# Performance work log

Hardware: AMD Instinct MI355X
Metric: run time of the kernel (lower is better)

The kernel has to match this reference:

```python
import jax, jax.numpy as jnp
import numpy as np

RADIUS = 0.2
NSAMPLE = 32
USE_XYZ = True


def setup_inputs() -> dict:
    key = jax.random.key(0)
    k1, k2, k3 = jax.random.split(key, 3)
    B, N, S, C = 8, 16384, 1024, 64
    xyz = jax.random.uniform(k1, (B, N, 3), dtype=jnp.float32)
    new_xyz = jax.random.uniform(k2, (B, S, 3), dtype=jnp.float32)
    features = jax.random.normal(k3, (B, C, N), dtype=jnp.float32)
    return {"xyz": xyz, "new_xyz": new_xyz, "features": features}


def _ball_query(xyz, new_xyz, radius, nsample):
    """For each query point, the first `nsample` point indices within `radius`,
    padded with the first valid index (0 if none) — matches the CUDA kernel."""
    B, N, _ = xyz.shape
    # squared distances [B, S, N]
    d2 = jnp.sum((new_xyz[:, :, None, :] - xyz[:, None, :, :]) ** 2, axis=-1)
    within = d2 < (radius * radius)
    # encode: valid points keep their index, invalid get sentinel N; sorting
    # then yields the first-in-order valid indices, as the CUDA kernel does.
    keys = jnp.where(within, jnp.arange(N, dtype=jnp.int32)[None, None, :], N)
    idx = jnp.sort(keys, axis=-1)[:, :, :nsample]          # [B, S, K]
    first = idx[:, :, 0:1]
    first = jnp.where(first < N, first, 0)                 # no neighbor -> 0
    idx = jnp.where(idx < N, idx, first)
    return idx.astype(jnp.int32)


def reference(xyz, new_xyz, features):
    idx = _ball_query(xyz, new_xyz, RADIUS, NSAMPLE)       # [B, S, K] int32
    # group xyz: gather [B, S, K, 3] then center on new_xyz
    grouped_xyz = jnp.take_along_axis(xyz[:, None, :, :], idx[:, :, :, None], axis=2)
    grouped_xyz = grouped_xyz - new_xyz[:, :, None, :]
    grouped_xyz = jnp.transpose(grouped_xyz, (0, 3, 1, 2))  # [B, 3, S, K]
    # group features: [B, C, 1, N] gathered with [B, 1, S, K] -> [B, C, S, K]
    grouped_feats = jnp.take_along_axis(features[:, :, :, None].transpose(0, 1, 3, 2),
                                        idx[:, None, :, :], axis=3)
    if USE_XYZ:
        return jnp.concatenate([grouped_xyz, grouped_feats], axis=1)  # [B, 3+C, S, K]
    return grouped_feats
```

## Files before the change

kernel.cpp:

```cpp
#include <hip/hip_runtime.h>


#define BB 8
#define NN 16384
#define SS 1024
#define CC 64
#define NSAMP 32
#define OUTCH (3 + CC)

#define R2 0.04f

__global__ __launch_bounds__(256) void query_kernel(
    const float* __restrict__ xyz,
    const float* __restrict__ new_xyz,
    int* __restrict__ idxq,
    float* __restrict__ out)
{
    __shared__ int sidx[4][NSAMP];

    const int t    = threadIdx.x;
    const int wave = t >> 6;
    const int lane = t & 63;
    const int q    = blockIdx.x * 4 + wave;
    const int b    = q >> 10;
    const int s    = q & (SS - 1);

    const float* xb = xyz + (size_t)b * NN * 3;
    const float qx = new_xyz[((size_t)b * SS + s) * 3 + 0];
    const float qy = new_xyz[((size_t)b * SS + s) * 3 + 1];
    const float qz = new_xyz[((size_t)b * SS + s) * 3 + 2];
    const unsigned long long below = (1ull << lane) - 1ull;

    int count = 0;
    for (int base = 0; base < NN; base += 512) {
        float d2[8];
        #pragma unroll
        for (int j = 0; j < 8; ++j) {
            const int i = base + j * 64 + lane;
            const float dx = qx - xb[i * 3 + 0];
            const float dy = qy - xb[i * 3 + 1];
            const float dz = qz - xb[i * 3 + 2];
            d2[j] = __fadd_rn(__fadd_rn(__fmul_rn(dx, dx),
                                        __fmul_rn(dy, dy)),
                              __fmul_rn(dz, dz));
        }
        #pragma unroll
        for (int j = 0; j < 8; ++j) {
            const bool within = d2[j] < R2;
            const unsigned long long m = __ballot(within);
            if (within) {
                const int pos = count + __popcll(m & below);
                if (pos < NSAMP) sidx[wave][pos] = base + j * 64 + lane;
            }
            count += __popcll(m);
        }
        if (count >= NSAMP) break;
    }
    __syncthreads();
    const int cnt = count < NSAMP ? count : NSAMP;
    const int first = (cnt > 0) ? sidx[wave][0] : 0;
    if (lane < NSAMP && lane >= cnt) sidx[wave][lane] = first;
    __syncthreads();

    if (lane < NSAMP) {
        const int k = lane;
        const int idx = sidx[wave][k];
        idxq[(size_t)q * NSAMP + k] = idx;
        const float gx = xb[idx * 3 + 0] - qx;
        const float gy = xb[idx * 3 + 1] - qy;
        const float gz = xb[idx * 3 + 2] - qz;
        const size_t o = (((size_t)b * OUTCH + 0) * SS + s) * NSAMP + k;
        out[o + 0 * (size_t)SS * NSAMP] = gx;
        out[o + 1 * (size_t)SS * NSAMP] = gy;
        out[o + 2 * (size_t)SS * NSAMP] = gz;
    }
}

__global__ __launch_bounds__(512) void gather_kernel(
    const float* __restrict__ feats,
    const int*   __restrict__ idxq,
    float* __restrict__ out)
{
    __shared__ float row[NN];

    const int c = blockIdx.x;
    const int b = blockIdx.y;
    const int t = threadIdx.x;

    const float* fr = feats + ((size_t)b * CC + c) * NN;
    #pragma unroll
    for (int i = 0; i < 8; ++i) {
        const int o = (i * 512 + t) * 4;
        *(float4*)(row + o) = *(const float4*)(fr + o);
    }
    __syncthreads();

    const int k4 = (t & 7) * 4;
    const int s0 = t >> 3;
    const int*  ib = idxq + (size_t)b * SS * NSAMP;
    float* ob = out + (((size_t)b * OUTCH + 3 + c) * SS) * NSAMP;
    #pragma unroll
    for (int it = 0; it < 16; ++it) {
        const int s = it * 64 + s0;
        const int4 id = *(const int4*)(ib + (size_t)s * NSAMP + k4);
        float4 v;
        v.x = row[id.x];
        v.y = row[id.y];
        v.z = row[id.z];
        v.w = row[id.w];
        *(float4*)(ob + (size_t)s * NSAMP + k4) = v;
    }
}

__global__ __launch_bounds__(64) void qg_fused(
    const float* __restrict__ xyz, const float* __restrict__ new_xyz,
    const float* __restrict__ feats, float* __restrict__ out)
{
    const int bs   = blockIdx.x;
    const int b    = bs >> 10;
    const int s    = bs & (SS - 1);
    const int lane = threadIdx.x;

    const float* xb = xyz + (size_t)b * NN * 3;
    const float qx = new_xyz[((size_t)b * SS + s) * 3 + 0];
    const float qy = new_xyz[((size_t)b * SS + s) * 3 + 1];
    const float qz = new_xyz[((size_t)b * SS + s) * 3 + 2];

    __shared__ int sidx[NSAMP];
    int count = 0;
    for (int base = 0; base < NN; base += 64) {
        const int i = base + lane;
        const float dx = qx - xb[i * 3 + 0];
        const float dy = qy - xb[i * 3 + 1];
        const float dz = qz - xb[i * 3 + 2];
        const float d2 = __fadd_rn(__fadd_rn(__fmul_rn(dx, dx),
                                             __fmul_rn(dy, dy)),
                                   __fmul_rn(dz, dz));
        const bool within = d2 < R2;
        const unsigned long long m = __ballot(within);
        if (within) {
            const int pos = count + __popcll(m & ((1ull << lane) - 1ull));
            if (pos < NSAMP) sidx[pos] = i;
        }
        count += __popcll(m);
        if (count >= NSAMP) break;
    }
    __syncthreads();
    const int cnt = count < NSAMP ? count : NSAMP;
    const int first = (cnt > 0) ? sidx[0] : 0;
    if (lane < NSAMP && lane >= cnt) sidx[lane] = first;
    __syncthreads();

    const int k    = lane & 31;
    const int half = lane >> 5;
    const int idx  = sidx[k];
    const size_t obase = (((size_t)b * OUTCH + 0) * SS + s) * NSAMP + k;
    if (half == 0) {
        out[obase + 0 * (size_t)SS * NSAMP] = xb[idx * 3 + 0] - qx;
        out[obase + 1 * (size_t)SS * NSAMP] = xb[idx * 3 + 1] - qy;
        out[obase + 2 * (size_t)SS * NSAMP] = xb[idx * 3 + 2] - qz;
    }
    const float* fb = feats + (size_t)b * CC * NN;
    const size_t fo = (((size_t)b * OUTCH + 3) * SS + s) * NSAMP + k;
    for (int cch = half; cch < CC; cch += 2) {
        out[fo + (size_t)cch * SS * NSAMP] = fb[(size_t)cch * NN + idx];
    }
}

extern "C" void kernel_launch(void* const* d_in, const int* in_sizes, int n_in,
                              void* d_out, int out_size, void* d_ws, size_t ws_size,
                              hipStream_t stream) {
    const float* xyz     = (const float*)d_in[0];
    const float* new_xyz = (const float*)d_in[1];
    const float* feats   = (const float*)d_in[2];
    float* out           = (float*)d_out;

    const size_t idx_bytes = (size_t)BB * SS * NSAMP * sizeof(int);

    if (ws_size >= idx_bytes) {
        int* idxq = (int*)d_ws;
        query_kernel<<<2048, 256, 0, stream>>>(xyz, new_xyz, idxq, out);
        gather_kernel<<<dim3(CC, BB), 512, 0, stream>>>(feats, idxq, out);
    } else {
        qg_fused<<<BB * SS, 64, 0, stream>>>(xyz, new_xyz, feats, out);
    }
}
```

Measured before the change: 115.4 us.

## Fuse ball query and feature gather into one kernel with per-batch atomic barrier

Merges the query and gather kernels into a single launch of 512 blocks. Each block first computes 16 ball queries for its batch while its feature row loads into registers, then signals a per-batch atomic counter and spin-waits until all 64 blocks of that batch finish before gathering. If the wait times out, the block recomputes all queries itself as a fallback. This drops one kernel launch and overlaps the feature loads with the query work. It relies on all blocks of a batch being co-resident, adds a memset and spin-wait cost, and swaps the popcount prefix for mbcnt.

```diff
diff --git a/kernel.cpp b/kernel.cpp
--- a/kernel.cpp
+++ b/kernel.cpp
@@ -7,30 +7,19 @@
 #define CC 64
 #define NSAMP 32
 #define OUTCH (3 + CC)
+#define GPB 64
+#define QPG 16
 
 #define R2 0.04f
 
-__global__ __launch_bounds__(256) void query_kernel(
-    const float* __restrict__ xyz,
-    const float* __restrict__ new_xyz,
+__device__ __forceinline__ void ball_query_one(
+    const float* __restrict__ xb,
+    const float qx, const float qy, const float qz,
+    const int b, const int s, const int lane,
+    int* __restrict__ swave,
     int* __restrict__ idxq,
     float* __restrict__ out)
 {
-    __shared__ int sidx[4][NSAMP];
-
-    const int t    = threadIdx.x;
-    const int wave = t >> 6;
-    const int lane = t & 63;
-    const int q    = blockIdx.x * 4 + wave;
-    const int b    = q >> 10;
-    const int s    = q & (SS - 1);
-
-    const float* xb = xyz + (size_t)b * NN * 3;
-    const float qx = new_xyz[((size_t)b * SS + s) * 3 + 0];
-    const float qy = new_xyz[((size_t)b * SS + s) * 3 + 1];
-    const float qz = new_xyz[((size_t)b * SS + s) * 3 + 2];
-    const unsigned long long below = (1ull << lane) - 1ull;
-
     int count = 0;
     for (int base = 0; base < NN; base += 512) {
         float d2[8];
@@ -49,23 +38,26 @@
             const bool within = d2[j] < R2;
             const unsigned long long m = __ballot(within);
             if (within) {
-                const int pos = count + __popcll(m & below);
-                if (pos < NSAMP) sidx[wave][pos] = base + j * 64 + lane;
+                const int pre = (int)__builtin_amdgcn_mbcnt_hi(
+                    (unsigned)(m >> 32),
+                    __builtin_amdgcn_mbcnt_lo((unsigned)m, 0u));
+                const int pos = count + pre;
+                if (pos < NSAMP) swave[pos] = base + j * 64 + lane;
             }
             count += __popcll(m);
         }
         if (count >= NSAMP) break;
     }
-    __syncthreads();
+    asm volatile("s_waitcnt lgkmcnt(0)" ::: "memory");
     const int cnt = count < NSAMP ? count : NSAMP;
-    const int first = (cnt > 0) ? sidx[wave][0] : 0;
-    if (lane < NSAMP && lane >= cnt) sidx[wave][lane] = first;
-    __syncthreads();
+    const int first = (cnt > 0) ? swave[0] : 0;
+    if (lane < NSAMP && lane >= cnt) swave[lane] = first;
+    asm volatile("s_waitcnt lgkmcnt(0)" ::: "memory");
 
     if (lane < NSAMP) {
         const int k = lane;
-        const int idx = sidx[wave][k];
-        idxq[(size_t)q * NSAMP + k] = idx;
+        const int idx = swave[k];
+        idxq[((size_t)b * SS + s) * NSAMP + k] = idx;
         const float gx = xb[idx * 3 + 0] - qx;
         const float gy = xb[idx * 3 + 1] - qy;
         const float gz = xb[idx * 3 + 2] - qz;
@@ -76,28 +68,74 @@
     }
 }
 
-__global__ __launch_bounds__(512) void gather_kernel(
+__global__ __launch_bounds__(512, 4) void fused_kernel(
+    const float* __restrict__ xyz,
+    const float* __restrict__ new_xyz,
     const float* __restrict__ feats,
-    const int*   __restrict__ idxq,
+    int*  __restrict__ idxq,
+    int*  __restrict__ done,
     float* __restrict__ out)
 {
     __shared__ float row[NN];
-
-    const int c = blockIdx.x;
-    const int b = blockIdx.y;
-    const int t = threadIdx.x;
+    __shared__ int   sidx[8][NSAMP];
+    __shared__ int   need_self;
+
+    const int t    = threadIdx.x;
+    const int wave = t >> 6;
+    const int lane = t & 63;
+    const int c    = blockIdx.x & (GPB - 1);
+    const int b    = blockIdx.x >> 6;
 
     const float* fr = feats + ((size_t)b * CC + c) * NN;
-    #pragma unroll
-    for (int i = 0; i < 8; ++i) {
-        const int o = (i * 512 + t) * 4;
-        *(float4*)(row + o) = *(const float4*)(fr + o);
-    }
-    __syncthreads();
+    float4 stg[8];
+    #pragma unroll
+    for (int i = 0; i < 8; ++i)
+        stg[i] = *(const float4*)(fr + (i * 512 + t) * 4);
+
+    const float* xb = xyz + (size_t)b * NN * 3;
+    const float* nb = new_xyz + (size_t)b * SS * 3;
+    #pragma unroll
+    for (int r = 0; r < 2; ++r) {
+        const int s = c * QPG + wave * 2 + r;
+        const float qx = nb[s * 3 + 0];
+        const float qy = nb[s * 3 + 1];
+        const float qz = nb[s * 3 + 2];
+        ball_query_one(xb, qx, qy, qz, b, s, lane, sidx[wave], idxq, out);
+    }
+    __syncthreads();
+    if (t == 0) {
+        __threadfence();
+        __hip_atomic_fetch_add(done + b, 1, __ATOMIC_RELEASE,
+                               __HIP_MEMORY_SCOPE_AGENT);
+    }
+
+    #pragma unroll
+    for (int i = 0; i < 8; ++i)
+        *(float4*)(row + (i * 512 + t) * 4) = stg[i];
+
+    if (t == 0) {
+        int ok = 1, spins = 0;
+        while (__hip_atomic_load(done + b, __ATOMIC_ACQUIRE,
+                                 __HIP_MEMORY_SCOPE_AGENT) < GPB) {
+            __builtin_amdgcn_s_sleep(2);
+            if (++spins > (1 << 20)) { ok = 0; break; }
+        }
+        need_self = ok ? 0 : 1;
+    }
+    __syncthreads();
+    if (need_self) {
+        for (int s = wave; s < SS; s += 8) {
+            const float qx = nb[s * 3 + 0];
+            const float qy = nb[s * 3 + 1];
+            const float qz = nb[s * 3 + 2];
+            ball_query_one(xb, qx, qy, qz, b, s, lane, sidx[wave], idxq, out);
+        }
+        __syncthreads();
+    }
 
     const int k4 = (t & 7) * 4;
     const int s0 = t >> 3;
-    const int*  ib = idxq + (size_t)b * SS * NSAMP;
+    const int* ib = idxq + (size_t)b * SS * NSAMP;
     float* ob = out + (((size_t)b * OUTCH + 3 + c) * SS) * NSAMP;
     #pragma unroll
     for (int it = 0; it < 16; ++it) {
@@ -175,12 +213,15 @@
     const float* feats   = (const float*)d_in[2];
     float* out           = (float*)d_out;
 
-    const size_t idx_bytes = (size_t)BB * SS * NSAMP * sizeof(int);
-
-    if (ws_size >= idx_bytes) {
+    const size_t idx_bytes  = (size_t)BB * SS * NSAMP * sizeof(int);
+    const size_t need_bytes = idx_bytes + BB * sizeof(int);
+
+    if (ws_size >= need_bytes) {
         int* idxq = (int*)d_ws;
-        query_kernel<<<2048, 256, 0, stream>>>(xyz, new_xyz, idxq, out);
-        gather_kernel<<<dim3(CC, BB), 512, 0, stream>>>(feats, idxq, out);
+        int* done = (int*)((char*)d_ws + idx_bytes);
+        hipMemsetAsync(done, 0, BB * sizeof(int), stream);
+        fused_kernel<<<BB * GPB, 512, 0, stream>>>(xyz, new_xyz, feats,
+                                                   idxq, done, out);
     } else {
         qg_fused<<<BB * SS, 64, 0, stream>>>(xyz, new_xyz, feats, out);
     }
```

New measurement: 200.5 us. 1.74x slower.
